# Kernel tuning notes

Hardware: AMD Instinct MI355X
Metric: run time of the kernel (lower is better)

## Reference

```python
import jax, jax.numpy as jnp
import numpy as np

EPS = 1e-5

def conv2d(x, w, b, stride, pad):
    y = jax.lax.conv_general_dilated(x, w, (stride, stride), [(pad, pad), (pad, pad)],
                                     dimension_numbers=('NCHW', 'OIHW', 'NCHW'))
    return y + b[None, :, None, None]

def _sample(xb, py, px):
    # xb: [C,H,W]; py,px: [K,Ho,Wo] fractional sample coords (zero padding outside)
    H, W = xb.shape[1], xb.shape[2]
    y0 = jnp.floor(py); x0 = jnp.floor(px)
    ay = py - y0; ax = px - x0
    y0i = y0.astype(jnp.int32); x0i = x0.astype(jnp.int32)
    out = jnp.zeros((xb.shape[0],) + py.shape, xb.dtype)
    for dy, wy in ((0, 1.0 - ay), (1, ay)):
        for dx, wx in ((0, 1.0 - ax), (1, ax)):
            yi = y0i + dy; xi = x0i + dx
            valid = (yi >= 0) & (yi < H) & (xi >= 0) & (xi < W)
            v = xb[:, jnp.clip(yi, 0, H - 1), jnp.clip(xi, 0, W - 1)]  # [C,K,Ho,Wo]
            out = out + v * (wy * wx * valid)[None]
    return out

def deform_conv2d(x, w, offset, mask, stride, pad):
    # torchvision.ops.deform_conv2d semantics (modulated, 1 offset group)
    B, C, H, W = x.shape
    Co, Ci, kh, kw = w.shape
    K = kh * kw
    Ho = (H + 2 * pad - kh) // stride + 1
    Wo = (W + 2 * pad - kw) // stride + 1
    ky, kx = jnp.meshgrid(jnp.arange(kh), jnp.arange(kw), indexing='ij')
    ky = ky.reshape(K).astype(x.dtype); kx = kx.reshape(K).astype(x.dtype)
    off = offset.reshape(B, K, 2, Ho, Wo)  # channel 2k = dy, 2k+1 = dx
    base_y = (jnp.arange(Ho) * stride - pad).astype(x.dtype)
    base_x = (jnp.arange(Wo) * stride - pad).astype(x.dtype)
    py = base_y[None, None, :, None] + ky[None, :, None, None] + off[:, :, 0]
    px = base_x[None, None, None, :] + kx[None, :, None, None] + off[:, :, 1]
    cols = jax.vmap(_sample)(x, py, px)        # [B,C,K,Ho,Wo]
    cols = cols * mask[:, None]                # modulated
    return jnp.einsum('bckhw,ock->bohw', cols, w.reshape(Co, Ci, K))

def deform_layer(x, off_w, off_b, mod_w, mod_b, w, stride, pad):
    offset = conv2d(x, off_w, off_b, stride, pad)
    mask = 2.0 * jax.nn.sigmoid(conv2d(x, mod_w, mod_b, stride, pad))
    return deform_conv2d(x, w, offset, mask, stride, pad)

def bn(x, g, b, m, v):
    return (x - m[None, :, None, None]) * (g / jnp.sqrt(v + EPS))[None, :, None, None] + b[None, :, None, None]

def prelu(x, alpha):
    return jnp.where(x > 0, x, alpha[None, :, None, None] * x)

def setup_inputs() -> dict:
    key = jax.random.key(0)
    ks = jax.random.split(key, 24)
    B, C, D, H, W, k = 4, 128, 128, 128, 128, 3
    K = k * k
    n = lambda i, shp, s: jax.random.normal(ks[i], shp, dtype=jnp.float32) * s
    inp = {
        'x': n(0, (B, C, H, W), 1.0),
        'bn1_g': 1.0 + n(1, (C,), 0.05), 'bn1_b': n(2, (C,), 0.05),
        'bn1_m': n(3, (C,), 0.1), 'bn1_v': jax.random.uniform(ks[4], (C,), jnp.float32, 0.5, 1.5),
        'off1_w': n(5, (2 * K, C, k, k), 0.01), 'off1_b': n(6, (2 * K,), 0.01),
        'mod1_w': n(7, (K, C, k, k), 0.01), 'mod1_b': n(8, (K,), 0.01),
        'w1': n(9, (D, C, k, k), 1.0 / np.sqrt(C * K)),
        'alpha': jnp.full((D,), 0.25, jnp.float32),
        'off2_w': n(10, (2 * K, D, k, k), 0.01), 'off2_b': n(11, (2 * K,), 0.01),
        'mod2_w': n(12, (K, D, k, k), 0.01), 'mod2_b': n(13, (K,), 0.01),
        'w2': n(14, (D, D, k, k), 1.0 / np.sqrt(D * K)),
        'bn2_g': 1.0 + n(15, (D,), 0.05), 'bn2_b': n(16, (D,), 0.05),
        'bn2_m': n(17, (D,), 0.1), 'bn2_v': jax.random.uniform(ks[18], (D,), jnp.float32, 0.5, 1.5),
    }
    return inp

def reference(x, bn1_g, bn1_b, bn1_m, bn1_v, off1_w, off1_b, mod1_w, mod1_b, w1, alpha,
              off2_w, off2_b, mod2_w, mod2_b, w2, bn2_g, bn2_b, bn2_m, bn2_v):
    # in_channel == depth, stride == 1 -> shortcut is MaxPool2d(1,1) == identity
    shortcut = x
    r = bn(x, bn1_g, bn1_b, bn1_m, bn1_v)
    r = deform_layer(r, off1_w, off1_b, mod1_w, mod1_b, w1, 1, 1)
    r = prelu(r, alpha)
    r = deform_layer(r, off2_w, off2_b, mod2_w, mod2_b, w2, 1, 1)
    r = bn(r, bn2_g, bn2_b, bn2_m, bn2_v)
    return r + shortcut
```

## Files before the change

### kernel.cpp

```cpp
#include <hip/hip_runtime.h>
#include <hip/hip_bf16.h>
#include <hip/hip_fp16.h>
#include <math.h>

#define DEV_INLINE __device__ __forceinline__

typedef __attribute__((ext_vector_type(8))) short short8;
typedef __attribute__((ext_vector_type(8))) unsigned short ushort8v;
typedef __attribute__((ext_vector_type(4))) float f32x4;

constexpr int H = 128, W = 128, C = 128, B = 4;
constexpr int KK = 9;
constexpr int KT2 = 1184;
constexpr int GP = 80;
constexpr int GHALF = 64 * GP;

DEV_INLINE unsigned short f2bf(float f) {
  union { float f; unsigned u; } v; v.f = f;
  unsigned r = v.u + 0x7FFFu + ((v.u >> 16) & 1u);
  return (unsigned short)(r >> 16);
}
DEV_INLINE float ubits(unsigned u) {
  union { unsigned u; float f; } v; v.u = u; return v.f;
}
DEV_INLINE unsigned pack2bf(float a, float b) {
  float2 t; t.x = a; t.y = b;
  __hip_bfloat162 h = __float22bfloat162_rn(t);
  union { __hip_bfloat162 h; unsigned u; } c; c.h = h;
  return c.u;
}
DEV_INLINE unsigned f2h2(float a, float b) {
  __half2 h = __floats2half2_rn(a, b);
  union { __half2 h; unsigned u; } c; c.h = h;
  return c.u;
}
DEV_INLINE float2 h2f2(unsigned u) {
  union { unsigned u; __half2 h; } c; c.u = u;
  return __half22float2(c.h);
}
DEV_INLINE unsigned blend4(unsigned TL, unsigned TR, unsigned BL, unsigned BR,
                           float w00, float w01, float w10, float w11) {
  const float lo = w00 * ubits(TL << 16) + w01 * ubits(TR << 16)
                 + w10 * ubits(BL << 16) + w11 * ubits(BR << 16);
  const float hi = w00 * ubits(TL & 0xFFFF0000u) + w01 * ubits(TR & 0xFFFF0000u)
                 + w10 * ubits(BL & 0xFFFF0000u) + w11 * ubits(BR & 0xFFFF0000u);
  return pack2bf(lo, hi);
}
DEV_INLINE void lgkm_barrier() {
  asm volatile("s_waitcnt lgkmcnt(0)" ::: "memory");
  __builtin_amdgcn_s_barrier();
  __builtin_amdgcn_sched_barrier(0);
}

template<int LAYER>
__global__ __launch_bounds__(256, 4)
void fusedL(const unsigned short* __restrict__ src,
            const unsigned short* __restrict__ wOM,
            const unsigned short* __restrict__ wS,
            const float* __restrict__ bias,
            const float* __restrict__ pA, const float* __restrict__ pB,
            const float* __restrict__ pM, const float* __restrict__ pV,
            const float* __restrict__ resid,
            unsigned short* __restrict__ outh,
            float* __restrict__ outf)
{
  constexpr bool BN   = (LAYER == 1);
  constexpr int  NCH3 = BN ? 37 : 36;
  __shared__ __attribute__((aligned(16))) char smem[17152];
  char* gBuf = smem;
  float* sOff = (float*)smem;
  unsigned* sTabU = (unsigned*)(smem + 10240);

  const int tid  = threadIdx.x;
  const int lane = tid & 63;
  const int m16  = lane & 15;
  const int q    = lane >> 4;
  const int wv   = tid >> 6;

  const int raw  = blockIdx.x;
  const int xcd  = raw & 7;
  const int slot = raw >> 3;
  const int b    = xcd >> 1;
  const int hy   = ((xcd & 1) << 6) | (slot >> 1);
  const int hx0  = (slot & 1) << 6;
  const unsigned short* __restrict__ srcB = src + ((size_t)b << 14) * C;

  const int pos  = (wv << 4) + m16;
  const int ppos = tid >> 2;
  const int ps   = tid & 3;

  f32x4 acc2[2];
  acc2[0] = (f32x4){0.f, 0.f, 0.f, 0.f};
  acc2[1] = (f32x4){0.f, 0.f, 0.f, 0.f};

  {
    const int iy = hy - 1, ix = hx0 + ppos - 1;
    uint4 v; v.x = 0; v.y = 0; v.z = 0; v.w = 0;
    if (((unsigned)iy < (unsigned)H) && ((unsigned)ix < (unsigned)W))
      v = *(const uint4*)(srcB + (size_t)(iy * W + ix) * C + (ps << 3));
    *(uint4*)(gBuf + ppos * GP + (ps << 4)) = v;
  }
  uint4 pendV; pendV.x = 0; pendV.y = 0; pendV.z = 0; pendV.w = 0;
  {
    const int iy = hy - 1, ix = hx0 + ppos - 1;
    if (((unsigned)iy < (unsigned)H) && ((unsigned)ix < (unsigned)W))
      pendV = *(const uint4*)(srcB + (size_t)(iy * W + ix) * C + 32 + (ps << 3));
  }
  short8 pa0 = *(const short8*)(wOM + (size_t)lane * 8);
  short8 pa1 = *(const short8*)(wOM + (size_t)lane * 8 + 512);
  lgkm_barrier();

  #pragma unroll 2
  for (int ch = 0; ch < 36; ++ch) {
    const int p = ch & 1;
    const short8 a0 = pa0, a1 = pa1;
    if (ch + 1 < 36) {
      const unsigned short* ap = wOM + ((size_t)((ch + 1) * 128 + lane)) * 8;
      pa0 = *(const short8*)(ap);
      pa1 = *(const short8*)(ap + 512);
    }
    uint4 newV; newV.x = 0; newV.y = 0; newV.z = 0; newV.w = 0;
    if (ch + 2 < 36) {
      const int t2 = (ch + 2) >> 2, c2 = (ch + 2) & 3;
      const int ky = t2 / 3, kx = t2 - 3 * (t2 / 3);
      const int iy = hy + ky - 1;
      const int ix = hx0 + ppos + kx - 1;
      if (((unsigned)iy < (unsigned)H) && ((unsigned)ix < (unsigned)W))
        newV = *(const uint4*)(srcB + (size_t)(iy * W + ix) * C + (c2 << 5) + (ps << 3));
    }
    if (ch + 1 < 36)
      *(uint4*)(gBuf + (p ^ 1) * GHALF + ppos * GP + (ps << 4)) = pendV;
    const short8 bfrg = *(const short8*)(gBuf + p * GHALF + pos * GP + (q << 4));
    acc2[0] = __builtin_amdgcn_mfma_f32_16x16x32_bf16(a0, bfrg, acc2[0], 0, 0, 0);
    acc2[1] = __builtin_amdgcn_mfma_f32_16x16x32_bf16(a1, bfrg, acc2[1], 0, 0, 0);
    pendV = newV;
    if (ch + 1 < 36) lgkm_barrier();
  }
  if constexpr (BN) {
    union { unsigned u[4]; short8 s; } bfr;
    float sv[8];
    #pragma unroll
    for (int j = 0; j < 8; ++j) {
      const int kj = (q << 3) + j;
      float s = 0.f;
      if (kj < KK) {
        const int ky = kj / 3, kx = kj - 3 * (kj / 3);
        const int iy = hy + ky - 1, ix = hx0 + pos + kx - 1;
        s = (((unsigned)iy < (unsigned)H) && ((unsigned)ix < (unsigned)W)) ? 1.f : 0.f;
      }
      sv[j] = s;
    }
    #pragma unroll
    for (int t = 0; t < 4; ++t) bfr.u[t] = pack2bf(sv[2 * t], sv[2 * t + 1]);
    const unsigned short* ap = wOM + ((size_t)36 * 128 + lane) * 8;
    acc2[0] = __builtin_amdgcn_mfma_f32_16x16x32_bf16(*(const short8*)(ap), bfr.s, acc2[0], 0, 0, 0);
    acc2[1] = __builtin_amdgcn_mfma_f32_16x16x32_bf16(*(const short8*)(ap + 512), bfr.s, acc2[1], 0, 0, 0);
  }
  __syncthreads();
  #pragma unroll
  for (int ot = 0; ot < 2; ++ot) {
    #pragma unroll
    for (int rg = 0; rg < 4; ++rg) {
      const int o = ot * 16 + (q << 2) + rg;
      if (o < 27) {
        float v = acc2[ot][rg] + bias[o];
        if (o >= 18) v = 2.f / (1.f + expf(-v));
        sOff[pos * 29 + o] = v;
      }
    }
  }
  __syncthreads();

  {
    const float* myOff = sOff + pos * 29;
    #pragma unroll
    for (int tap = 0; tap < 9; ++tap) {
      const int ky = tap / 3, kx = tap - 3 * (tap / 3);
      const float oy = myOff[2 * tap];
      const float ox = myOff[2 * tap + 1];
      const float mv = myOff[18 + tap];
      const float py = (float)(hy - 1 + ky) + oy;
      const float px = (float)(hx0 + pos - 1 + kx) + ox;
      const float fy = floorf(py), fx = floorf(px);
      const float ay = py - fy, ax = px - fx;
      const int y0 = (int)fy, x0 = (int)fx;
      const int y1 = y0 + 1, x1 = x0 + 1;
      const float wyt = (1.f - ay) * (((unsigned)y0 < (unsigned)H) ? 1.f : 0.f);
      const float wyb = ay * (((unsigned)y1 < (unsigned)H) ? 1.f : 0.f);
      const int y0c = min(max(y0, 0), H - 1), y1c = min(max(y1, 0), H - 1);
      const int bx  = min(max(x0, 0), W - 2);
      float wA = 0.f, wB = 0.f;
      if (x0 == bx)          { wA = 1.f - ax; wB = ax; }
      else if (x1 == bx)     { wA = ax; }
      else if (x0 == bx + 1) { wB = 1.f - ax; }
      if (q == 0) {
        const int tb = (tap * 64 + pos) * 3;
        sTabU[tb + 0] = (unsigned)(y0c * W + bx) | ((unsigned)(y1c * W + bx) << 16);
        sTabU[tb + 1] = f2h2(mv * wyt * wA, mv * wyt * wB);
        sTabU[tb + 2] = f2h2(mv * wyb * wA, mv * wyb * wB);
      }
    }
  }
  __syncthreads();

  f32x4 acc[2][4];
  #pragma unroll
  for (int i = 0; i < 2; ++i)
    #pragma unroll
    for (int j = 0; j < 4; ++j) acc[i][j] = (f32x4){0.f, 0.f, 0.f, 0.f};

  unsigned tabId, tabW0, tabW1;
  {
    const int tb = ppos * 3;
    tabId = sTabU[tb]; tabW0 = sTabU[tb + 1]; tabW1 = sTabU[tb + 2];
  }
  {
    const unsigned short* pT  = srcB + (size_t)(tabId & 0xFFFFu) * C + (ps << 3);
    const unsigned short* pBm = srcB + (size_t)(tabId >> 16) * C + (ps << 3);
    const uint4 TL = *(const uint4*)(pT),  TR = *(const uint4*)(pT + C);
    const uint4 BL = *(const uint4*)(pBm), BR = *(const uint4*)(pBm + C);
    const float2 wa = h2f2(tabW0), wb = h2f2(tabW1);
    uint4 o;
    o.x = blend4(TL.x, TR.x, BL.x, BR.x, wa.x, wa.y, wb.x, wb.y);
    o.y = blend4(TL.y, TR.y, BL.y, BR.y, wa.x, wa.y, wb.x, wb.y);
    o.z = blend4(TL.z, TR.z, BL.z, BR.z, wa.x, wa.y, wb.x, wb.y);
    o.w = blend4(TL.w, TR.w, BL.w, BR.w, wa.x, wa.y, wb.x, wb.y);
    *(uint4*)(gBuf + ppos * GP + (ps << 4)) = o;
  }
  uint4 pTL, pTR, pBL, pBR;
  {
    const int cbn = 32 + (ps << 3);
    const unsigned short* pT  = srcB + (size_t)(tabId & 0xFFFFu) * C + cbn;
    const unsigned short* pBm = srcB + (size_t)(tabId >> 16) * C + cbn;
    pTL = *(const uint4*)(pT);  pTR = *(const uint4*)(pT + C);
    pBL = *(const uint4*)(pBm); pBR = *(const uint4*)(pBm + C);
  }
  short8 pa0_, pa1_;
  {
    const unsigned short* ap = wS + ((size_t)((2 * wv) * 64 + lane)) * 8;
    pa0_ = *(const short8*)(ap);
    pa1_ = *(const short8*)(ap + 512);
  }
  lgkm_barrier();

  #pragma unroll 2
  for (int ch = 0; ch < 36; ++ch) {
    const int p = ch & 1;
    const short8 af0 = pa0_, af1 = pa1_;
    if (ch + 1 < NCH3) {
      const unsigned short* ap = wS + ((size_t)((ch + 1) * 4096)) +
                                 ((size_t)((2 * wv) * 64 + lane)) * 8;
      pa0_ = *(const short8*)(ap);
      pa1_ = *(const short8*)(ap + 512);
    }
    unsigned ntId = tabId, ntW0 = tabW0, ntW1 = tabW1;
    if ((((ch + 2) & 3) == 0) && (ch + 2 < 36)) {
      const int tb = (((ch + 2) >> 2) * 64 + ppos) * 3;
      ntId = sTabU[tb]; ntW0 = sTabU[tb + 1]; ntW1 = sTabU[tb + 2];
    }
    uint4 nTL = pTL, nTR = pTR, nBL = pBL, nBR = pBR;
    if (ch + 2 < 36) {
      const int cbn = (((ch + 2) & 3) << 5) + (ps << 3);
      const unsigned short* pT  = srcB + (size_t)(ntId & 0xFFFFu) * C + cbn;
      const unsigned short* pBm = srcB + (size_t)(ntId >> 16) * C + cbn;
      nTL = *(const uint4*)(pT);  nTR = *(const uint4*)(pT + C);
      nBL = *(const uint4*)(pBm); nBR = *(const uint4*)(pBm + C);
    }
    if (ch + 1 < 36) {
      const float2 wa = h2f2(tabW0), wb = h2f2(tabW1);
      uint4 o;
      o.x = blend4(pTL.x, pTR.x, pBL.x, pBR.x, wa.x, wa.y, wb.x, wb.y);
      o.y = blend4(pTL.y, pTR.y, pBL.y, pBR.y, wa.x, wa.y, wb.x, wb.y);
      o.z = blend4(pTL.z, pTR.z, pBL.z, pBR.z, wa.x, wa.y, wb.x, wb.y);
      o.w = blend4(pTL.w, pTR.w, pBL.w, pBR.w, wa.x, wa.y, wb.x, wb.y);
      *(uint4*)(gBuf + (p ^ 1) * GHALF + ppos * GP + (ps << 4)) = o;
    }
    const char* gb = gBuf + p * GHALF;
    short8 bf[4];
    #pragma unroll
    for (int pg = 0; pg < 4; ++pg)
      bf[pg] = *(const short8*)(gb + (pg * 16 + m16) * GP + (q << 4));
    #pragma unroll
    for (int pg = 0; pg < 4; ++pg) {
      acc[0][pg] = __builtin_amdgcn_mfma_f32_16x16x32_bf16(af0, bf[pg], acc[0][pg], 0, 0, 0);
      acc[1][pg] = __builtin_amdgcn_mfma_f32_16x16x32_bf16(af1, bf[pg], acc[1][pg], 0, 0, 0);
    }
    pTL = nTL; pTR = nTR; pBL = nBL; pBR = nBR;
    tabId = ntId; tabW0 = ntW0; tabW1 = ntW1;
    if (ch + 1 < 36) lgkm_barrier();
  }

  if constexpr (BN) {
    const short8 af0 = pa0_, af1 = pa1_;
    #pragma unroll
    for (int pg = 0; pg < 4; ++pg) {
      float sv[8];
      #pragma unroll
      for (int j = 0; j < 8; ++j) {
        const int k = (q << 3) + j;
        float s = 0.f;
        if (k < KK) {
          const int tb = (k * 64 + pg * 16 + m16) * 3;
          const float2 a = h2f2(sTabU[tb + 1]);
          const float2 c = h2f2(sTabU[tb + 2]);
          s = a.x + a.y + c.x + c.y;
        }
        sv[j] = s;
      }
      union { unsigned u[4]; short8 s; } bfr;
      #pragma unroll
      for (int t = 0; t < 4; ++t) bfr.u[t] = pack2bf(sv[2 * t], sv[2 * t + 1]);
      acc[0][pg] = __builtin_amdgcn_mfma_f32_16x16x32_bf16(af0, bfr.s, acc[0][pg], 0, 0, 0);
      acc[1][pg] = __builtin_amdgcn_mfma_f32_16x16x32_bf16(af1, bfr.s, acc[1][pg], 0, 0, 0);
    }
  }

  #pragma unroll
  for (int oi = 0; oi < 2; ++oi) {
    const int ot = wv * 2 + oi;
    if constexpr (LAYER == 1) {
      const float a0 = pA[ot * 16 + (q << 2) + 0];
      const float a1 = pA[ot * 16 + (q << 2) + 1];
      const float a2 = pA[ot * 16 + (q << 2) + 2];
      const float a3 = pA[ot * 16 + (q << 2) + 3];
      #pragma unroll
      for (int pg = 0; pg < 4; ++pg) {
        const float v0 = acc[oi][pg][0], v1 = acc[oi][pg][1];
        const float v2 = acc[oi][pg][2], v3 = acc[oi][pg][3];
        uint2 st;
        st.x = pack2bf(v0 > 0.f ? v0 : a0 * v0, v1 > 0.f ? v1 : a1 * v1);
        st.y = pack2bf(v2 > 0.f ? v2 : a2 * v2, v3 > 0.f ? v3 : a3 * v3);
        const int n = (b << 14) + hy * W + hx0 + pg * 16 + m16;
        *(uint2*)(outh + (size_t)n * C + ot * 16 + (q << 2)) = st;
      }
    } else {
      #pragma unroll
      for (int rg = 0; rg < 4; ++rg) {
        const int o = ot * 16 + (q << 2) + rg;
        const float s  = pA[o] * rsqrtf(pV[o] + 1e-5f);
        const float sh = pB[o] - pM[o] * s;
        #pragma unroll
        for (int pg = 0; pg < 4; ++pg) {
          const size_t oi2 = (((size_t)(b * C + o)) << 14) + hy * W + hx0 + pg * 16 + m16;
          outf[oi2] = acc[oi][pg][rg] * s + sh + resid[oi2];
        }
      }
    }
  }
}

__global__ __launch_bounds__(256, 4)
void xcvt3(const float* __restrict__ x, unsigned short* __restrict__ xb)
{
  __shared__ unsigned tile[64 * 69];
  const int b   = blockIdx.y;
  const int p0  = blockIdx.x * 64;
  const int tid = threadIdx.x;
  const int pl  = tid & 63;
  const int cg  = tid >> 6;
  const float* __restrict__ xp = x + (((size_t)(b * C) + cg * 32) << 14) + p0 + pl;
  #pragma unroll
  for (int j = 0; j < 16; ++j) {
    const float a = xp[(size_t)(2 * j) << 14];
    const float c = xp[(size_t)(2 * j + 1) << 14];
    tile[pl * 69 + cg * 16 + j] = pack2bf(a, c);
  }
  __syncthreads();
  const int pl2 = tid >> 2;
  const int cq  = tid & 3;
  unsigned* dst = (unsigned*)(xb + (((size_t)(b << 14)) + p0 + pl2) * C + cq * 32);
  #pragma unroll
  for (int k = 0; k < 16; k += 4) {
    uint4 v;
    v.x = tile[pl2 * 69 + cq * 16 + k];
    v.y = tile[pl2 * 69 + cq * 16 + k + 1];
    v.z = tile[pl2 * 69 + cq * 16 + k + 2];
    v.w = tile[pl2 * 69 + cq * 16 + k + 3];
    *(uint4*)(dst + k) = v;
  }
}

__global__ void prep5(const float* __restrict__ w1, const float* __restrict__ w2,
                      const float* __restrict__ ow1, const float* __restrict__ mw1,
                      const float* __restrict__ ob1, const float* __restrict__ mb1,
                      const float* __restrict__ ow2, const float* __restrict__ mw2,
                      const float* __restrict__ ob2, const float* __restrict__ mb2,
                      const float* __restrict__ g, const float* __restrict__ bb,
                      const float* __restrict__ m, const float* __restrict__ v,
                      unsigned short* __restrict__ wb1, unsigned short* __restrict__ wb2,
                      unsigned short* __restrict__ wom1, unsigned short* __restrict__ wom2,
                      float* __restrict__ bias1, float* __restrict__ bias2)
{
  const int i = blockIdx.x * 256 + threadIdx.x;
  if (i < 128 * KT2) {
    const int j = i & 7, lane = (i >> 3) & 63, ot = (i >> 9) & 7, ch = i >> 12;
    const int o = ot * 16 + (lane & 15);
    const int qj = ((lane >> 4) << 3) + j;
    unsigned short v1 = 0, v2 = 0;
    if (ch < 36) {
      const int tap = ch >> 2;
      const int c   = ((ch & 3) << 5) + qj;
      const float s = g[c] * rsqrtf(v[c] + 1e-5f);
      v1 = f2bf(w1[(size_t)(o * 128 + c) * 9 + tap] * s);
      v2 = f2bf(w2[(size_t)(o * 128 + c) * 9 + tap]);
    } else if (qj < KK) {
      float acc = 0.f;
      for (int c = 0; c < 128; ++c) {
        const float s  = g[c] * rsqrtf(v[c] + 1e-5f);
        const float sh = bb[c] - m[c] * s;
        acc += w1[(size_t)(o * 128 + c) * 9 + qj] * sh;
      }
      v1 = f2bf(acc);
    }
    wb1[i] = v1; wb2[i] = v2;
  }
  if (i < 32 * KT2) {
    const int j = i & 7, lane = (i >> 3) & 63, ot = (i >> 9) & 1, ch = i >> 10;
    const int o = ot * 16 + (lane & 15);
    const int qj = ((lane >> 4) << 3) + j;
    unsigned short v1 = 0, v2 = 0;
    if (ch < 36) {
      const int tap = ch >> 2;
      const int c   = ((ch & 3) << 5) + qj;
      const float s = g[c] * rsqrtf(v[c] + 1e-5f);
      if (o < 18) {
        v1 = f2bf(ow1[(size_t)(o * 128 + c) * 9 + tap] * s);
        v2 = f2bf(ow2[(size_t)(o * 128 + c) * 9 + tap]);
      } else if (o < 27) {
        v1 = f2bf(mw1[(size_t)((o - 18) * 128 + c) * 9 + tap] * s);
        v2 = f2bf(mw2[(size_t)((o - 18) * 128 + c) * 9 + tap]);
      }
    } else if (qj < KK && o < 27) {
      const float* wsrc = (o < 18) ? ow1 + (size_t)o * 1152
                                   : mw1 + (size_t)(o - 18) * 1152;
      float acc = 0.f;
      for (int c = 0; c < 128; ++c) {
        const float s  = g[c] * rsqrtf(v[c] + 1e-5f);
        const float sh = bb[c] - m[c] * s;
        acc += wsrc[(size_t)c * 9 + qj] * sh;
      }
      v1 = f2bf(acc);
    }
    wom1[i] = v1; wom2[i] = v2;
  }
  if (i < 32) {
    float b1 = 0.f, b2 = 0.f;
    if (i < 18)      { b1 = ob1[i];      b2 = ob2[i]; }
    else if (i < 27) { b1 = mb1[i - 18]; b2 = mb2[i - 18]; }
    bias1[i] = b1; bias2[i] = b2;
  }
}

extern "C" void kernel_launch(void* const* d_in, const int* in_sizes, int n_in,
                              void* d_out, int out_size, void* d_ws, size_t ws_size,
                              hipStream_t stream)
{
  const float* x     = (const float*)d_in[0];
  const float* bn1g  = (const float*)d_in[1];
  const float* bn1b  = (const float*)d_in[2];
  const float* bn1m  = (const float*)d_in[3];
  const float* bn1v  = (const float*)d_in[4];
  const float* ow1   = (const float*)d_in[5];
  const float* ob1   = (const float*)d_in[6];
  const float* mw1   = (const float*)d_in[7];
  const float* mb1   = (const float*)d_in[8];
  const float* w1    = (const float*)d_in[9];
  const float* alpha = (const float*)d_in[10];
  const float* ow2   = (const float*)d_in[11];
  const float* ob2   = (const float*)d_in[12];
  const float* mw2   = (const float*)d_in[13];
  const float* mb2   = (const float*)d_in[14];
  const float* w2    = (const float*)d_in[15];
  const float* bn2g  = (const float*)d_in[16];
  const float* bn2b  = (const float*)d_in[17];
  const float* bn2m  = (const float*)d_in[18];
  const float* bn2v  = (const float*)d_in[19];
  float* out = (float*)d_out;

  char* wsp = (char*)d_ws;
  unsigned short* xbf  = (unsigned short*)(wsp);
  unsigned short* r2bf = (unsigned short*)(wsp + 16777216);
  unsigned short* wb1  = (unsigned short*)(wsp + 40632320);
  unsigned short* wb2  = (unsigned short*)(wsp + 40935424);
  unsigned short* wom1 = (unsigned short*)(wsp + 41238528);
  unsigned short* wom2 = (unsigned short*)(wsp + 41314304);
  float* bias1 = (float*)(wsp + 41390080);
  float* bias2 = (float*)(wsp + 41390208);

  xcvt3<<<dim3(256, 4), 256, 0, stream>>>(x, xbf);
  prep5<<<(128 * KT2 + 255) / 256, 256, 0, stream>>>(
      w1, w2, ow1, mw1, ob1, mb1, ow2, mw2, ob2, mb2,
      bn1g, bn1b, bn1m, bn1v, wb1, wb2, wom1, wom2, bias1, bias2);

  fusedL<1><<<1024, 256, 0, stream>>>(xbf, wom1, wb1, bias1, alpha,
      nullptr, nullptr, nullptr, nullptr, r2bf, nullptr);
  fusedL<2><<<1024, 256, 0, stream>>>(r2bf, wom2, wb2, bias2, bn2g,
      bn2b, bn2m, bn2v, x, nullptr, out);
}
```

Before: 257.7 us.

## Halve pixel tile per block to 32 and raise occupancy to 6 waves

Each fused deformable-conv block now covers 32 output pixels instead of 64. The grid doubles to 2048 blocks and shared memory per block is halved. The offset-conv phase splits its two output-channel tiles across wave pairs, and the main GEMM uses a 2x2 accumulator set per wave instead of 2x4. The goal is more resident blocks per CU to hide gather latency, at the cost of narrower (8-byte) loads, less weight reuse per block, and only 32 threads building the sampling table.

```diff
diff --git a/kernel.cpp b/kernel.cpp
--- a/kernel.cpp
+++ b/kernel.cpp
@@ -13,7 +13,7 @@
 constexpr int KK = 9;
 constexpr int KT2 = 1184;
 constexpr int GP = 80;
-constexpr int GHALF = 64 * GP;
+constexpr int GHALF = 32 * GP;
 
 DEV_INLINE unsigned short f2bf(float f) {
   union { float f; unsigned u; } v; v.f = f;
@@ -53,7 +53,7 @@
 }
 
 template<int LAYER>
-__global__ __launch_bounds__(256, 4)
+__global__ __launch_bounds__(256, 6)
 void fusedL(const unsigned short* __restrict__ src,
             const unsigned short* __restrict__ wOM,
             const unsigned short* __restrict__ wS,
@@ -66,10 +66,10 @@
 {
   constexpr bool BN   = (LAYER == 1);
   constexpr int  NCH3 = BN ? 37 : 36;
-  __shared__ __attribute__((aligned(16))) char smem[17152];
+  __shared__ __attribute__((aligned(16))) char smem[8576];
   char* gBuf = smem;
   float* sOff = (float*)smem;
-  unsigned* sTabU = (unsigned*)(smem + 10240);
+  unsigned* sTabU = (unsigned*)(smem + 5120);
 
   const int tid  = threadIdx.x;
   const int lane = tid & 63;
@@ -81,58 +81,54 @@
   const int xcd  = raw & 7;
   const int slot = raw >> 3;
   const int b    = xcd >> 1;
-  const int hy   = ((xcd & 1) << 6) | (slot >> 1);
-  const int hx0  = (slot & 1) << 6;
+  const int hy   = ((xcd & 1) << 6) | (slot >> 2);
+  const int hx0  = (slot & 3) << 5;
   const unsigned short* __restrict__ srcB = src + ((size_t)b << 14) * C;
 
-  const int pos  = (wv << 4) + m16;
-  const int ppos = tid >> 2;
-  const int ps   = tid & 3;
-
-  f32x4 acc2[2];
-  acc2[0] = (f32x4){0.f, 0.f, 0.f, 0.f};
-  acc2[1] = (f32x4){0.f, 0.f, 0.f, 0.f};
+  const int pgw  = wv & 1;
+  const int ntw  = wv >> 1;
+  const int pos1 = (pgw << 4) + m16;
+  const int ppos = tid >> 3;
+  const int ps8  = tid & 7;
+
+  f32x4 acc2 = (f32x4){0.f, 0.f, 0.f, 0.f};
 
   {
     const int iy = hy - 1, ix = hx0 + ppos - 1;
-    uint4 v; v.x = 0; v.y = 0; v.z = 0; v.w = 0;
+    uint2 v; v.x = 0; v.y = 0;
     if (((unsigned)iy < (unsigned)H) && ((unsigned)ix < (unsigned)W))
-      v = *(const uint4*)(srcB + (size_t)(iy * W + ix) * C + (ps << 3));
-    *(uint4*)(gBuf + ppos * GP + (ps << 4)) = v;
-  }
-  uint4 pendV; pendV.x = 0; pendV.y = 0; pendV.z = 0; pendV.w = 0;
+      v = *(const uint2*)(srcB + (size_t)(iy * W + ix) * C + (ps8 << 2));
+    *(uint2*)(gBuf + ppos * GP + (ps8 << 3)) = v;
+  }
+  uint2 pendV; pendV.x = 0; pendV.y = 0;
   {
     const int iy = hy - 1, ix = hx0 + ppos - 1;
     if (((unsigned)iy < (unsigned)H) && ((unsigned)ix < (unsigned)W))
-      pendV = *(const uint4*)(srcB + (size_t)(iy * W + ix) * C + 32 + (ps << 3));
-  }
-  short8 pa0 = *(const short8*)(wOM + (size_t)lane * 8);
-  short8 pa1 = *(const short8*)(wOM + (size_t)lane * 8 + 512);
+      pendV = *(const uint2*)(srcB + (size_t)(iy * W + ix) * C + 32 + (ps8 << 2));
+  }
+  short8 pa0 = *(const short8*)(wOM + ((size_t)(ntw * 64 + lane)) * 8);
   lgkm_barrier();
 
   #pragma unroll 2
   for (int ch = 0; ch < 36; ++ch) {
     const int p = ch & 1;
-    const short8 a0 = pa0, a1 = pa1;
+    const short8 a0 = pa0;
     if (ch + 1 < 36) {
-      const unsigned short* ap = wOM + ((size_t)((ch + 1) * 128 + lane)) * 8;
-      pa0 = *(const short8*)(ap);
-      pa1 = *(const short8*)(ap + 512);
-    }
-    uint4 newV; newV.x = 0; newV.y = 0; newV.z = 0; newV.w = 0;
+      pa0 = *(const short8*)(wOM + ((size_t)((ch + 1) * 128 + ntw * 64 + lane)) * 8);
+    }
+    uint2 newV; newV.x = 0; newV.y = 0;
     if (ch + 2 < 36) {
       const int t2 = (ch + 2) >> 2, c2 = (ch + 2) & 3;
       const int ky = t2 / 3, kx = t2 - 3 * (t2 / 3);
       const int iy = hy + ky - 1;
       const int ix = hx0 + ppos + kx - 1;
       if (((unsigned)iy < (unsigned)H) && ((unsigned)ix < (unsigned)W))
-        newV = *(const uint4*)(srcB + (size_t)(iy * W + ix) * C + (c2 << 5) + (ps << 3));
+        newV = *(const uint2*)(srcB + (size_t)(iy * W + ix) * C + (c2 << 5) + (ps8 << 2));
     }
     if (ch + 1 < 36)
-      *(uint4*)(gBuf + (p ^ 1) * GHALF + ppos * GP + (ps << 4)) = pendV;
-    const short8 bfrg = *(const short8*)(gBuf + p * GHALF + pos * GP + (q << 4));
-    acc2[0] = __builtin_amdgcn_mfma_f32_16x16x32_bf16(a0, bfrg, acc2[0], 0, 0, 0);
-    acc2[1] = __builtin_amdgcn_mfma_f32_16x16x32_bf16(a1, bfrg, acc2[1], 0, 0, 0);
+      *(uint2*)(gBuf + (p ^ 1) * GHALF + ppos * GP + (ps8 << 3)) = pendV;
+    const short8 bfrg = *(const short8*)(gBuf + p * GHALF + pos1 * GP + (q << 4));
+    acc2 = __builtin_amdgcn_mfma_f32_16x16x32_bf16(a0, bfrg, acc2, 0, 0, 0);
     pendV = newV;
     if (ch + 1 < 36) lgkm_barrier();
   }
@@ -145,34 +141,30 @@
       float s = 0.f;
       if (kj < KK) {
         const int ky = kj / 3, kx = kj - 3 * (kj / 3);
-        const int iy = hy + ky - 1, ix = hx0 + pos + kx - 1;
+        const int iy = hy + ky - 1, ix = hx0 + pos1 + kx - 1;
         s = (((unsigned)iy < (unsigned)H) && ((unsigned)ix < (unsigned)W)) ? 1.f : 0.f;
       }
       sv[j] = s;
     }
     #pragma unroll
     for (int t = 0; t < 4; ++t) bfr.u[t] = pack2bf(sv[2 * t], sv[2 * t + 1]);
-    const unsigned short* ap = wOM + ((size_t)36 * 128 + lane) * 8;
-    acc2[0] = __builtin_amdgcn_mfma_f32_16x16x32_bf16(*(const short8*)(ap), bfr.s, acc2[0], 0, 0, 0);
-    acc2[1] = __builtin_amdgcn_mfma_f32_16x16x32_bf16(*(const short8*)(ap + 512), bfr.s, acc2[1], 0, 0, 0);
+    const short8 a36 = *(const short8*)(wOM + ((size_t)(36 * 128 + ntw * 64 + lane)) * 8);
+    acc2 = __builtin_amdgcn_mfma_f32_16x16x32_bf16(a36, bfr.s, acc2, 0, 0, 0);
   }
   __syncthreads();
   #pragma unroll
-  for (int ot = 0; ot < 2; ++ot) {
-    #pragma unroll
-    for (int rg = 0; rg < 4; ++rg) {
-      const int o = ot * 16 + (q << 2) + rg;
-      if (o < 27) {
-        float v = acc2[ot][rg] + bias[o];
-        if (o >= 18) v = 2.f / (1.f + expf(-v));
-        sOff[pos * 29 + o] = v;
-      }
+  for (int rg = 0; rg < 4; ++rg) {
+    const int o = ntw * 16 + (q << 2) + rg;
+    if (o < 27) {
+      float v = acc2[rg] + bias[o];
+      if (o >= 18) v = 2.f / (1.f + expf(-v));
+      sOff[pos1 * 29 + o] = v;
     }
   }
   __syncthreads();
 
-  {
-    const float* myOff = sOff + pos * 29;
+  if (tid < 32) {
+    const float* myOff = sOff + tid * 29;
     #pragma unroll
     for (int tap = 0; tap < 9; ++tap) {
       const int ky = tap / 3, kx = tap - 3 * (tap / 3);
@@ -180,7 +172,7 @@
       const float ox = myOff[2 * tap + 1];
       const float mv = myOff[18 + tap];
       const float py = (float)(hy - 1 + ky) + oy;
-      const float px = (float)(hx0 + pos - 1 + kx) + ox;
+      const float px = (float)(hx0 + tid - 1 + kx) + ox;
       const float fy = floorf(py), fx = floorf(px);
       const float ay = py - fy, ax = px - fx;
       const int y0 = (int)fy, x0 = (int)fx;
@@ -193,21 +185,19 @@
       if (x0 == bx)          { wA = 1.f - ax; wB = ax; }
       else if (x1 == bx)     { wA = ax; }
       else if (x0 == bx + 1) { wB = 1.f - ax; }
-      if (q == 0) {
-        const int tb = (tap * 64 + pos) * 3;
-        sTabU[tb + 0] = (unsigned)(y0c * W + bx) | ((unsigned)(y1c * W + bx) << 16);
-        sTabU[tb + 1] = f2h2(mv * wyt * wA, mv * wyt * wB);
-        sTabU[tb + 2] = f2h2(mv * wyb * wA, mv * wyb * wB);
-      }
+      const int tb = (tap * 32 + tid) * 3;
+      sTabU[tb + 0] = (unsigned)(y0c * W + bx) | ((unsigned)(y1c * W + bx) << 16);
+      sTabU[tb + 1] = f2h2(mv * wyt * wA, mv * wyt * wB);
+      sTabU[tb + 2] = f2h2(mv * wyb * wA, mv * wyb * wB);
     }
   }
   __syncthreads();
 
-  f32x4 acc[2][4];
+  f32x4 acc[2][2];
   #pragma unroll
   for (int i = 0; i < 2; ++i)
     #pragma unroll
-    for (int j = 0; j < 4; ++j) acc[i][j] = (f32x4){0.f, 0.f, 0.f, 0.f};
+    for (int j = 0; j < 2; ++j) acc[i][j] = (f32x4){0.f, 0.f, 0.f, 0.f};
 
   unsigned tabId, tabW0, tabW1;
   {
@@ -215,25 +205,24 @@
     tabId = sTabU[tb]; tabW0 = sTabU[tb + 1]; tabW1 = sTabU[tb + 2];
   }
   {
-    const unsigned short* pT  = srcB + (size_t)(tabId & 0xFFFFu) * C + (ps << 3);
-    const unsigned short* pBm = srcB + (size_t)(tabId >> 16) * C + (ps << 3);
-    const uint4 TL = *(const uint4*)(pT),  TR = *(const uint4*)(pT + C);
-    const uint4 BL = *(const uint4*)(pBm), BR = *(const uint4*)(pBm + C);
+    const int cbn = ps8 << 2;
+    const unsigned short* pT  = srcB + (size_t)(tabId & 0xFFFFu) * C + cbn;
+    const unsigned short* pBm = srcB + (size_t)(tabId >> 16) * C + cbn;
+    const uint2 TL = *(const uint2*)(pT),  TR = *(const uint2*)(pT + C);
+    const uint2 BL = *(const uint2*)(pBm), BR = *(const uint2*)(pBm + C);
     const float2 wa = h2f2(tabW0), wb = h2f2(tabW1);
-    uint4 o;
+    uint2 o;
     o.x = blend4(TL.x, TR.x, BL.x, BR.x, wa.x, wa.y, wb.x, wb.y);
     o.y = blend4(TL.y, TR.y, BL.y, BR.y, wa.x, wa.y, wb.x, wb.y);
-    o.z = blend4(TL.z, TR.z, BL.z, BR.z, wa.x, wa.y, wb.x, wb.y);
-    o.w = blend4(TL.w, TR.w, BL.w, BR.w, wa.x, wa.y, wb.x, wb.y);
-    *(uint4*)(gBuf + ppos * GP + (ps << 4)) = o;
-  }
-  uint4 pTL, pTR, pBL, pBR;
-  {
-    const int cbn = 32 + (ps << 3);
+    *(uint2*)(gBuf + ppos * GP + (ps8 << 3)) = o;
+  }
+  uint2 pTL, pTR, pBL, pBR;
+  {
+    const int cbn = 32 + (ps8 << 2);
     const unsigned short* pT  = srcB + (size_t)(tabId & 0xFFFFu) * C + cbn;
     const unsigned short* pBm = srcB + (size_t)(tabId >> 16) * C + cbn;
-    pTL = *(const uint4*)(pT);  pTR = *(const uint4*)(pT + C);
-    pBL = *(const uint4*)(pBm); pBR = *(const uint4*)(pBm + C);
+    pTL = *(const uint2*)(pT);  pTR = *(const uint2*)(pT + C);
+    pBL = *(const uint2*)(pBm); pBR = *(const uint2*)(pBm + C);
   }
   short8 pa0_, pa1_;
   {
@@ -255,36 +244,31 @@
     }
     unsigned ntId = tabId, ntW0 = tabW0, ntW1 = tabW1;
     if ((((ch + 2) & 3) == 0) && (ch + 2 < 36)) {
-      const int tb = (((ch + 2) >> 2) * 64 + ppos) * 3;
+      const int tb = (((ch + 2) >> 2) * 32 + ppos) * 3;
       ntId = sTabU[tb]; ntW0 = sTabU[tb + 1]; ntW1 = sTabU[tb + 2];
     }
-    uint4 nTL = pTL, nTR = pTR, nBL = pBL, nBR = pBR;
+    uint2 nTL = pTL, nTR = pTR, nBL = pBL, nBR = pBR;
     if (ch + 2 < 36) {
-      const int cbn = (((ch + 2) & 3) << 5) + (ps << 3);
+      const int cbn = (((ch + 2) & 3) << 5) + (ps8 << 2);
       const unsigned short* pT  = srcB + (size_t)(ntId & 0xFFFFu) * C + cbn;
       const unsigned short* pBm = srcB + (size_t)(ntId >> 16) * C + cbn;
-      nTL = *(const uint4*)(pT);  nTR = *(const uint4*)(pT + C);
-      nBL = *(const uint4*)(pBm); nBR = *(const uint4*)(pBm + C);
+      nTL = *(const uint2*)(pT);  nTR = *(const uint2*)(pT + C);
+      nBL = *(const uint2*)(pBm); nBR = *(const uint2*)(pBm + C);
     }
     if (ch + 1 < 36) {
       const float2 wa = h2f2(tabW0), wb = h2f2(tabW1);
-      uint4 o;
+      uint2 o;
       o.x = blend4(pTL.x, pTR.x, pBL.x, pBR.x, wa.x, wa.y, wb.x, wb.y);
       o.y = blend4(pTL.y, pTR.y, pBL.y, pBR.y, wa.x, wa.y, wb.x, wb.y);
-      o.z = blend4(pTL.z, pTR.z, pBL.z, pBR.z, wa.x, wa.y, wb.x, wb.y);
-      o.w = blend4(pTL.w, pTR.w, pBL.w, pBR.w, wa.x, wa.y, wb.x, wb.y);
-      *(uint4*)(gBuf + (p ^ 1) * GHALF + ppos * GP + (ps << 4)) = o;
+      *(uint2*)(gBuf + (p ^ 1) * GHALF + ppos * GP + (ps8 << 3)) = o;
     }
     const char* gb = gBuf + p * GHALF;
-    short8 bf[4];
-    #pragma unroll
-    for (int pg = 0; pg < 4; ++pg)
-      bf[pg] = *(const short8*)(gb + (pg * 16 + m16) * GP + (q << 4));
-    #pragma unroll
-    for (int pg = 0; pg < 4; ++pg) {
-      acc[0][pg] = __builtin_amdgcn_mfma_f32_16x16x32_bf16(af0, bf[pg], acc[0][pg], 0, 0, 0);
-      acc[1][pg] = __builtin_amdgcn_mfma_f32_16x16x32_bf16(af1, bf[pg], acc[1][pg], 0, 0, 0);
-    }
+    const short8 bf0 = *(const short8*)(gb + m16 * GP + (q << 4));
+    const short8 bf1 = *(const short8*)(gb + (16 + m16) * GP + (q << 4));
+    acc[0][0] = __builtin_amdgcn_mfma_f32_16x16x32_bf16(af0, bf0, acc[0][0], 0, 0, 0);
+    acc[0][1] = __builtin_amdgcn_mfma_f32_16x16x32_bf16(af0, bf1, acc[0][1], 0, 0, 0);
+    acc[1][0] = __builtin_amdgcn_mfma_f32_16x16x32_bf16(af1, bf0, acc[1][0], 0, 0, 0);
+    acc[1][1] = __builtin_amdgcn_mfma_f32_16x16x32_bf16(af1, bf1, acc[1][1], 0, 0, 0);
     pTL = nTL; pTR = nTR; pBL = nBL; pBR = nBR;
     tabId = ntId; tabW0 = ntW0; tabW1 = ntW1;
     if (ch + 1 < 36) lgkm_barrier();
@@ -293,14 +277,14 @@
   if constexpr (BN) {
     const short8 af0 = pa0_, af1 = pa1_;
     #pragma unroll
-    for (int pg = 0; pg < 4; ++pg) {
+    for (int pg = 0; pg < 2; ++pg) {
       float sv[8];
       #pragma unroll
       for (int j = 0; j < 8; ++j) {
         const int k = (q << 3) + j;
         float s = 0.f;
         if (k < KK) {
-          const int tb = (k * 64 + pg * 16 + m16) * 3;
+          const int tb = (k * 32 + pg * 16 + m16) * 3;
           const float2 a = h2f2(sTabU[tb + 1]);
           const float2 c = h2f2(sTabU[tb + 2]);
           s = a.x + a.y + c.x + c.y;
@@ -324,7 +308,7 @@
       const float a2 = pA[ot * 16 + (q << 2) + 2];
       const float a3 = pA[ot * 16 + (q << 2) + 3];
       #pragma unroll
-      for (int pg = 0; pg < 4; ++pg) {
+      for (int pg = 0; pg < 2; ++pg) {
         const float v0 = acc[oi][pg][0], v1 = acc[oi][pg][1];
         const float v2 = acc[oi][pg][2], v3 = acc[oi][pg][3];
         uint2 st;
@@ -340,7 +324,7 @@
         const float s  = pA[o] * rsqrtf(pV[o] + 1e-5f);
         const float sh = pB[o] - pM[o] * s;
         #pragma unroll
-        for (int pg = 0; pg < 4; ++pg) {
+        for (int pg = 0; pg < 2; ++pg) {
           const size_t oi2 = (((size_t)(b * C + o)) << 14) + hy * W + hx0 + pg * 16 + m16;
           outf[oi2] = acc[oi][pg][rg] * s + sh + resid[oi2];
         }
@@ -492,8 +476,8 @@
       w1, w2, ow1, mw1, ob1, mb1, ow2, mw2, ob2, mb2,
       bn1g, bn1b, bn1m, bn1v, wb1, wb2, wom1, wom2, bias1, bias2);
 
-  fusedL<1><<<1024, 256, 0, stream>>>(xbf, wom1, wb1, bias1, alpha,
+  fusedL<1><<<2048, 256, 0, stream>>>(xbf, wom1, wb1, bias1, alpha,
       nullptr, nullptr, nullptr, nullptr, r2bf, nullptr);
-  fusedL<2><<<1024, 256, 0, stream>>>(r2bf, wom2, wb2, bias2, bn2g,
+  fusedL<2><<<2048, 256, 0, stream>>>(r2bf, wom2, wb2, bias2, bn2g,
       bn2b, bn2m, bn2v, x, nullptr, out);
 }
```

After: 299.0 us. 16.0% more time.

## Process two K-chunks per barrier with four-slot LDS ring in both GEMM phases

Applied to the files above, without the earlier changes.

Both main loops (offset/mask conv and deformable sampling GEMM) now handle two 32-channel chunks per iteration, using four LDS slots instead of a two-slot double buffer. This halves the number of block-wide barriers and gives global loads a longer prefetch distance. Weight fragments are now loaded inside the iteration rather than register-prefetched one step ahead. The cost is more LDS per block (27 KB vs 17 KB), which may reduce occupancy, and higher register pressure from holding eight bilinear corner vectors.

```diff
diff --git a/kernel.cpp b/kernel.cpp
--- a/kernel.cpp
+++ b/kernel.cpp
@@ -13,7 +13,7 @@
 constexpr int KK = 9;
 constexpr int KT2 = 1184;
 constexpr int GP = 80;
-constexpr int GHALF = 64 * GP;
+constexpr int GSLOT = 64 * GP;
 
 DEV_INLINE unsigned short f2bf(float f) {
   union { float f; unsigned u; } v; v.f = f;
@@ -64,12 +64,11 @@
             unsigned short* __restrict__ outh,
             float* __restrict__ outf)
 {
-  constexpr bool BN   = (LAYER == 1);
-  constexpr int  NCH3 = BN ? 37 : 36;
-  __shared__ __attribute__((aligned(16))) char smem[17152];
+  constexpr bool BN = (LAYER == 1);
+  __shared__ __attribute__((aligned(16))) char smem[27392];
   char* gBuf = smem;
   float* sOff = (float*)smem;
-  unsigned* sTabU = (unsigned*)(smem + 10240);
+  unsigned* sTabU = (unsigned*)(smem + 20480);
 
   const int tid  = threadIdx.x;
   const int lane = tid & 63;
@@ -95,46 +94,61 @@
 
   {
     const int iy = hy - 1, ix = hx0 + ppos - 1;
-    uint4 v; v.x = 0; v.y = 0; v.z = 0; v.w = 0;
-    if (((unsigned)iy < (unsigned)H) && ((unsigned)ix < (unsigned)W))
-      v = *(const uint4*)(srcB + (size_t)(iy * W + ix) * C + (ps << 3));
-    *(uint4*)(gBuf + ppos * GP + (ps << 4)) = v;
-  }
-  uint4 pendV; pendV.x = 0; pendV.y = 0; pendV.z = 0; pendV.w = 0;
+    const bool ok = ((unsigned)iy < (unsigned)H) && ((unsigned)ix < (unsigned)W);
+    #pragma unroll
+    for (int c = 0; c < 2; ++c) {
+      uint4 v; v.x = 0; v.y = 0; v.z = 0; v.w = 0;
+      if (ok) v = *(const uint4*)(srcB + (size_t)(iy * W + ix) * C + (c << 5) + (ps << 3));
+      *(uint4*)(gBuf + c * GSLOT + ppos * GP + (ps << 4)) = v;
+    }
+  }
+  uint4 Q0, Q1;
+  Q0.x = 0; Q0.y = 0; Q0.z = 0; Q0.w = 0; Q1 = Q0;
   {
     const int iy = hy - 1, ix = hx0 + ppos - 1;
-    if (((unsigned)iy < (unsigned)H) && ((unsigned)ix < (unsigned)W))
-      pendV = *(const uint4*)(srcB + (size_t)(iy * W + ix) * C + 32 + (ps << 3));
-  }
-  short8 pa0 = *(const short8*)(wOM + (size_t)lane * 8);
-  short8 pa1 = *(const short8*)(wOM + (size_t)lane * 8 + 512);
+    if (((unsigned)iy < (unsigned)H) && ((unsigned)ix < (unsigned)W)) {
+      Q0 = *(const uint4*)(srcB + (size_t)(iy * W + ix) * C + (2 << 5) + (ps << 3));
+      Q1 = *(const uint4*)(srcB + (size_t)(iy * W + ix) * C + (3 << 5) + (ps << 3));
+    }
+  }
   lgkm_barrier();
 
   #pragma unroll 2
-  for (int ch = 0; ch < 36; ++ch) {
-    const int p = ch & 1;
-    const short8 a0 = pa0, a1 = pa1;
-    if (ch + 1 < 36) {
-      const unsigned short* ap = wOM + ((size_t)((ch + 1) * 128 + lane)) * 8;
-      pa0 = *(const short8*)(ap);
-      pa1 = *(const short8*)(ap + 512);
-    }
-    uint4 newV; newV.x = 0; newV.y = 0; newV.z = 0; newV.w = 0;
-    if (ch + 2 < 36) {
-      const int t2 = (ch + 2) >> 2, c2 = (ch + 2) & 3;
-      const int ky = t2 / 3, kx = t2 - 3 * (t2 / 3);
+  for (int i = 0; i < 18; ++i) {
+    const int c0   = 2 * i;
+    const int cons = (i & 1) ? 2 : 0;
+    const int wsl  = (i & 1) ? 0 : 2;
+    const unsigned short* apA = wOM + ((size_t)(c0 * 128 + lane)) * 8;
+    const unsigned short* apB = wOM + ((size_t)((c0 + 1) * 128 + lane)) * 8;
+    const short8 a00 = *(const short8*)(apA);
+    const short8 a01 = *(const short8*)(apA + 512);
+    const short8 a10 = *(const short8*)(apB);
+    const short8 a11 = *(const short8*)(apB + 512);
+    if (c0 + 2 < 36) {
+      *(uint4*)(gBuf + wsl * GSLOT + ppos * GP + (ps << 4)) = Q0;
+      *(uint4*)(gBuf + (wsl + 1) * GSLOT + ppos * GP + (ps << 4)) = Q1;
+    }
+    if (c0 + 4 < 36) {
+      const int t4 = (c0 + 4) >> 2;
+      const int ky = t4 / 3, kx = t4 - 3 * (t4 / 3);
       const int iy = hy + ky - 1;
       const int ix = hx0 + ppos + kx - 1;
-      if (((unsigned)iy < (unsigned)H) && ((unsigned)ix < (unsigned)W))
-        newV = *(const uint4*)(srcB + (size_t)(iy * W + ix) * C + (c2 << 5) + (ps << 3));
-    }
-    if (ch + 1 < 36)
-      *(uint4*)(gBuf + (p ^ 1) * GHALF + ppos * GP + (ps << 4)) = pendV;
-    const short8 bfrg = *(const short8*)(gBuf + p * GHALF + pos * GP + (q << 4));
-    acc2[0] = __builtin_amdgcn_mfma_f32_16x16x32_bf16(a0, bfrg, acc2[0], 0, 0, 0);
-    acc2[1] = __builtin_amdgcn_mfma_f32_16x16x32_bf16(a1, bfrg, acc2[1], 0, 0, 0);
-    pendV = newV;
-    if (ch + 1 < 36) lgkm_barrier();
+      const bool ok = ((unsigned)iy < (unsigned)H) && ((unsigned)ix < (unsigned)W);
+      uint4 z; z.x = 0; z.y = 0; z.z = 0; z.w = 0;
+      Q0 = z; Q1 = z;
+      if (ok) {
+        const unsigned short* sp = srcB + (size_t)(iy * W + ix) * C + (ps << 3);
+        Q0 = *(const uint4*)(sp + (((c0 + 4) & 3) << 5));
+        Q1 = *(const uint4*)(sp + (((c0 + 5) & 3) << 5));
+      }
+    }
+    const short8 bf0 = *(const short8*)(gBuf + cons * GSLOT + pos * GP + (q << 4));
+    const short8 bf1 = *(const short8*)(gBuf + (cons + 1) * GSLOT + pos * GP + (q << 4));
+    acc2[0] = __builtin_amdgcn_mfma_f32_16x16x32_bf16(a00, bf0, acc2[0], 0, 0, 0);
+    acc2[1] = __builtin_amdgcn_mfma_f32_16x16x32_bf16(a01, bf0, acc2[1], 0, 0, 0);
+    acc2[0] = __builtin_amdgcn_mfma_f32_16x16x32_bf16(a10, bf1, acc2[0], 0, 0, 0);
+    acc2[1] = __builtin_amdgcn_mfma_f32_16x16x32_bf16(a11, bf1, acc2[1], 0, 0, 0);
+    if (i < 17) lgkm_barrier();
   }
   if constexpr (BN) {
     union { unsigned u[4]; short8 s; } bfr;
@@ -209,89 +223,112 @@
     #pragma unroll
     for (int j = 0; j < 4; ++j) acc[i][j] = (f32x4){0.f, 0.f, 0.f, 0.f};
 
-  unsigned tabId, tabW0, tabW1;
+  unsigned tI_id, tI_w0, tI_w1;
   {
     const int tb = ppos * 3;
-    tabId = sTabU[tb]; tabW0 = sTabU[tb + 1]; tabW1 = sTabU[tb + 2];
-  }
-  {
-    const unsigned short* pT  = srcB + (size_t)(tabId & 0xFFFFu) * C + (ps << 3);
-    const unsigned short* pBm = srcB + (size_t)(tabId >> 16) * C + (ps << 3);
-    const uint4 TL = *(const uint4*)(pT),  TR = *(const uint4*)(pT + C);
-    const uint4 BL = *(const uint4*)(pBm), BR = *(const uint4*)(pBm + C);
-    const float2 wa = h2f2(tabW0), wb = h2f2(tabW1);
-    uint4 o;
-    o.x = blend4(TL.x, TR.x, BL.x, BR.x, wa.x, wa.y, wb.x, wb.y);
-    o.y = blend4(TL.y, TR.y, BL.y, BR.y, wa.x, wa.y, wb.x, wb.y);
-    o.z = blend4(TL.z, TR.z, BL.z, BR.z, wa.x, wa.y, wb.x, wb.y);
-    o.w = blend4(TL.w, TR.w, BL.w, BR.w, wa.x, wa.y, wb.x, wb.y);
-    *(uint4*)(gBuf + ppos * GP + (ps << 4)) = o;
-  }
-  uint4 pTL, pTR, pBL, pBR;
-  {
-    const int cbn = 32 + (ps << 3);
-    const unsigned short* pT  = srcB + (size_t)(tabId & 0xFFFFu) * C + cbn;
-    const unsigned short* pBm = srcB + (size_t)(tabId >> 16) * C + cbn;
-    pTL = *(const uint4*)(pT);  pTR = *(const uint4*)(pT + C);
-    pBL = *(const uint4*)(pBm); pBR = *(const uint4*)(pBm + C);
-  }
-  short8 pa0_, pa1_;
-  {
-    const unsigned short* ap = wS + ((size_t)((2 * wv) * 64 + lane)) * 8;
-    pa0_ = *(const short8*)(ap);
-    pa1_ = *(const short8*)(ap + 512);
+    tI_id = sTabU[tb]; tI_w0 = sTabU[tb + 1]; tI_w1 = sTabU[tb + 2];
+  }
+  {
+    const float2 wa = h2f2(tI_w0), wb = h2f2(tI_w1);
+    #pragma unroll
+    for (int c = 0; c < 2; ++c) {
+      const int cbn = (c << 5) + (ps << 3);
+      const unsigned short* pT  = srcB + (size_t)(tI_id & 0xFFFFu) * C + cbn;
+      const unsigned short* pBm = srcB + (size_t)(tI_id >> 16) * C + cbn;
+      const uint4 TL = *(const uint4*)(pT),  TR = *(const uint4*)(pT + C);
+      const uint4 BL = *(const uint4*)(pBm), BR = *(const uint4*)(pBm + C);
+      uint4 o;
+      o.x = blend4(TL.x, TR.x, BL.x, BR.x, wa.x, wa.y, wb.x, wb.y);
+      o.y = blend4(TL.y, TR.y, BL.y, BR.y, wa.x, wa.y, wb.x, wb.y);
+      o.z = blend4(TL.z, TR.z, BL.z, BR.z, wa.x, wa.y, wb.x, wb.y);
+      o.w = blend4(TL.w, TR.w, BL.w, BR.w, wa.x, wa.y, wb.x, wb.y);
+      *(uint4*)(gBuf + c * GSLOT + ppos * GP + (ps << 4)) = o;
+    }
+  }
+  uint4 P0TL, P0TR, P0BL, P0BR, P1TL, P1TR, P1BL, P1BR;
+  {
+    const unsigned short* rT  = srcB + (size_t)(tI_id & 0xFFFFu) * C + (ps << 3);
+    const unsigned short* rB  = srcB + (size_t)(tI_id >> 16) * C + (ps << 3);
+    P0TL = *(const uint4*)(rT + 64);      P0TR = *(const uint4*)(rT + 64 + C);
+    P0BL = *(const uint4*)(rB + 64);      P0BR = *(const uint4*)(rB + 64 + C);
+    P1TL = *(const uint4*)(rT + 96);      P1TR = *(const uint4*)(rT + 96 + C);
+    P1BL = *(const uint4*)(rB + 96);      P1BR = *(const uint4*)(rB + 96 + C);
+  }
+  unsigned tB_w0 = tI_w0, tB_w1 = tI_w1;
+  {
+    const int tb = (64 + ppos) * 3;
+    tI_id = sTabU[tb]; tI_w0 = sTabU[tb + 1]; tI_w1 = sTabU[tb + 2];
   }
   lgkm_barrier();
 
   #pragma unroll 2
-  for (int ch = 0; ch < 36; ++ch) {
-    const int p = ch & 1;
-    const short8 af0 = pa0_, af1 = pa1_;
-    if (ch + 1 < NCH3) {
-      const unsigned short* ap = wS + ((size_t)((ch + 1) * 4096)) +
-                                 ((size_t)((2 * wv) * 64 + lane)) * 8;
-      pa0_ = *(const short8*)(ap);
-      pa1_ = *(const short8*)(ap + 512);
-    }
-    unsigned ntId = tabId, ntW0 = tabW0, ntW1 = tabW1;
-    if ((((ch + 2) & 3) == 0) && (ch + 2 < 36)) {
-      const int tb = (((ch + 2) >> 2) * 64 + ppos) * 3;
-      ntId = sTabU[tb]; ntW0 = sTabU[tb + 1]; ntW1 = sTabU[tb + 2];
-    }
-    uint4 nTL = pTL, nTR = pTR, nBL = pBL, nBR = pBR;
-    if (ch + 2 < 36) {
-      const int cbn = (((ch + 2) & 3) << 5) + (ps << 3);
-      const unsigned short* pT  = srcB + (size_t)(ntId & 0xFFFFu) * C + cbn;
-      const unsigned short* pBm = srcB + (size_t)(ntId >> 16) * C + cbn;
-      nTL = *(const uint4*)(pT);  nTR = *(const uint4*)(pT + C);
-      nBL = *(const uint4*)(pBm); nBR = *(const uint4*)(pBm + C);
-    }
-    if (ch + 1 < 36) {
-      const float2 wa = h2f2(tabW0), wb = h2f2(tabW1);
+  for (int i = 0; i < 18; ++i) {
+    const int c0   = 2 * i;
+    const int cons = (i & 1) ? 2 : 0;
+    const int wsl  = (i & 1) ? 0 : 2;
+    const unsigned short* apA = wS + (size_t)c0 * 4096 +
+                                ((size_t)((2 * wv) * 64 + lane)) * 8;
+    const unsigned short* apB = apA + 4096;
+    const short8 afA0 = *(const short8*)(apA);
+    const short8 afA1 = *(const short8*)(apA + 512);
+    const short8 afB0 = *(const short8*)(apB);
+    const short8 afB1 = *(const short8*)(apB + 512);
+    if (c0 + 2 < 36) {
+      const float2 wa = h2f2(tB_w0), wb = h2f2(tB_w1);
       uint4 o;
-      o.x = blend4(pTL.x, pTR.x, pBL.x, pBR.x, wa.x, wa.y, wb.x, wb.y);
-      o.y = blend4(pTL.y, pTR.y, pBL.y, pBR.y, wa.x, wa.y, wb.x, wb.y);
-      o.z = blend4(pTL.z, pTR.z, pBL.z, pBR.z, wa.x, wa.y, wb.x, wb.y);
-      o.w = blend4(pTL.w, pTR.w, pBL.w, pBR.w, wa.x, wa.y, wb.x, wb.y);
-      *(uint4*)(gBuf + (p ^ 1) * GHALF + ppos * GP + (ps << 4)) = o;
-    }
-    const char* gb = gBuf + p * GHALF;
+      o.x = blend4(P0TL.x, P0TR.x, P0BL.x, P0BR.x, wa.x, wa.y, wb.x, wb.y);
+      o.y = blend4(P0TL.y, P0TR.y, P0BL.y, P0BR.y, wa.x, wa.y, wb.x, wb.y);
+      o.z = blend4(P0TL.z, P0TR.z, P0BL.z, P0BR.z, wa.x, wa.y, wb.x, wb.y);
+      o.w = blend4(P0TL.w, P0TR.w, P0BL.w, P0BR.w, wa.x, wa.y, wb.x, wb.y);
+      *(uint4*)(gBuf + wsl * GSLOT + ppos * GP + (ps << 4)) = o;
+      o.x = blend4(P1TL.x, P1TR.x, P1BL.x, P1BR.x, wa.x, wa.y, wb.x, wb.y);
+      o.y = blend4(P1TL.y, P1TR.y, P1BL.y, P1BR.y, wa.x, wa.y, wb.x, wb.y);
+      o.z = blend4(P1TL.z, P1TR.z, P1BL.z, P1BR.z, wa.x, wa.y, wb.x, wb.y);
+      o.w = blend4(P1TL.w, P1TR.w, P1BL.w, P1BR.w, wa.x, wa.y, wb.x, wb.y);
+      *(uint4*)(gBuf + (wsl + 1) * GSLOT + ppos * GP + (ps << 4)) = o;
+    }
+    if (c0 + 4 < 36) {
+      const unsigned short* rT = srcB + (size_t)(tI_id & 0xFFFFu) * C + (ps << 3);
+      const unsigned short* rB = srcB + (size_t)(tI_id >> 16) * C + (ps << 3);
+      const int b0 = (((c0 + 4) & 3) << 5);
+      const int b1 = (((c0 + 5) & 3) << 5);
+      P0TL = *(const uint4*)(rT + b0);  P0TR = *(const uint4*)(rT + b0 + C);
+      P0BL = *(const uint4*)(rB + b0);  P0BR = *(const uint4*)(rB + b0 + C);
+      P1TL = *(const uint4*)(rT + b1);  P1TR = *(const uint4*)(rT + b1 + C);
+      P1BL = *(const uint4*)(rB + b1);  P1BR = *(const uint4*)(rB + b1 + C);
+    }
+    tB_w0 = tI_w0; tB_w1 = tI_w1;
+    if ((i & 1) && (c0 + 6 < 36)) {
+      const int tb = (((i + 3) >> 1) * 64 + ppos) * 3;
+      tI_id = sTabU[tb]; tI_w0 = sTabU[tb + 1]; tI_w1 = sTabU[tb + 2];
+    }
+    const char* gbA = gBuf + cons * GSLOT;
+    const char* gbB = gBuf + (cons + 1) * GSLOT;
     short8 bf[4];
     #pragma unroll
     for (int pg = 0; pg < 4; ++pg)
-      bf[pg] = *(const short8*)(gb + (pg * 16 + m16) * GP + (q << 4));
+      bf[pg] = *(const short8*)(gbA + (pg * 16 + m16) * GP + (q << 4));
     #pragma unroll
     for (int pg = 0; pg < 4; ++pg) {
-      acc[0][pg] = __builtin_amdgcn_mfma_f32_16x16x32_bf16(af0, bf[pg], acc[0][pg], 0, 0, 0);
-      acc[1][pg] = __builtin_amdgcn_mfma_f32_16x16x32_bf16(af1, bf[pg], acc[1][pg], 0, 0, 0);
-    }
-    pTL = nTL; pTR = nTR; pBL = nBL; pBR = nBR;
-    tabId = ntId; tabW0 = ntW0; tabW1 = ntW1;
-    if (ch + 1 < 36) lgkm_barrier();
+      acc[0][pg] = __builtin_amdgcn_mfma_f32_16x16x32_bf16(afA0, bf[pg], acc[0][pg], 0, 0, 0);
+      acc[1][pg] = __builtin_amdgcn_mfma_f32_16x16x32_bf16(afA1, bf[pg], acc[1][pg], 0, 0, 0);
+    }
+    #pragma unroll
+    for (int pg = 0; pg < 4; ++pg)
+      bf[pg] = *(const short8*)(gbB + (pg * 16 + m16) * GP + (q << 4));
+    #pragma unroll
+    for (int pg = 0; pg < 4; ++pg) {
+      acc[0][pg] = __builtin_amdgcn_mfma_f32_16x16x32_bf16(afB0, bf[pg], acc[0][pg], 0, 0, 0);
+      acc[1][pg] = __builtin_amdgcn_mfma_f32_16x16x32_bf16(afB1, bf[pg], acc[1][pg], 0, 0, 0);
+    }
+    if (i < 17) lgkm_barrier();
   }
 
   if constexpr (BN) {
-    const short8 af0 = pa0_, af1 = pa1_;
+    const unsigned short* ap = wS + (size_t)36 * 4096 +
+                               ((size_t)((2 * wv) * 64 + lane)) * 8;
+    const short8 af0 = *(const short8*)(ap);
+    const short8 af1 = *(const short8*)(ap + 512);
     #pragma unroll
     for (int pg = 0; pg < 4; ++pg) {
       float sv[8];
```

Measured after the change: 245.9 us. -4.6%, faster.
